# Kernel optimization log

Hardware: AMD Instinct MI355X
Metric: run time of the kernel (lower is better)

## Reference

```python
import jax, jax.numpy as jnp
import numpy as np

MAX_LEN, BATCH, EMB = 512, 32, 41
HID, UNITS = 800, 20
BOND_LENS = jnp.array([1.329, 1.459, 1.525], jnp.float32)
BOND_ANGLES = jnp.array([2.034, 2.119, 1.937], jnp.float32)
INIT_ABC = jnp.array([[0.0, 0.0, 1.0], [0.0, 1.0, 0.0], [1.0, 0.0, 0.0]], jnp.float32)


def _lstm_dir(x, w_ih, w_hh, b, reverse):
    # x: [T, B, in]; returns hidden states [T, B, H]
    T, B, _ = x.shape
    H = w_hh.shape[1]
    xs = jnp.flip(x, 0) if reverse else x
    xw = jnp.einsum('tbi,gi->tbg', xs, w_ih) + b  # precompute input projection

    def step(carry, xt):
        h, c = carry
        gates = xt + h @ w_hh.T
        i, f, g, o = jnp.split(gates, 4, axis=-1)
        c = jax.nn.sigmoid(f) * c + jax.nn.sigmoid(i) * jnp.tanh(g)
        h = jax.nn.sigmoid(o) * jnp.tanh(c)
        return (h, c), h

    init = (jnp.zeros((B, H), x.dtype), jnp.zeros((B, H), x.dtype))
    _, hs = jax.lax.scan(step, init, xw)
    return jnp.flip(hs, 0) if reverse else hs


def _bilstm_layer(x, w_ih, w_hh, b):
    # w_ih: [2, 4H, in]; w_hh: [2, 4H, H]; b: [2, 4H]
    fwd = _lstm_dir(x, w_ih[0], w_hh[0], b[0], False)
    bwd = _lstm_dir(x, w_ih[1], w_hh[1], b[1], True)
    return jnp.concatenate([fwd, bwd], axis=-1)


def _geometric_unit(coords3, triplet):
    # coords3: [3, B, 3] last three atoms; triplet: [B, 3] torsion angles
    A, Bc, C = coords3[0], coords3[1], coords3[2]
    new = []
    for i in range(3):
        Tang, R, P = BOND_ANGLES[i], BOND_LENS[i], triplet[:, i]
        D2 = jnp.stack([-R * jnp.cos(Tang) * jnp.ones_like(P),
                        R * jnp.cos(P) * jnp.sin(Tang),
                        R * jnp.sin(P) * jnp.sin(Tang)], axis=1)  # [B,3]
        BC = C - Bc
        bc = BC / jnp.linalg.norm(BC, axis=1, keepdims=True)
        AB = Bc - A
        N = jnp.cross(AB, bc)
        n = N / jnp.linalg.norm(N, axis=1, keepdims=True)
        M = jnp.stack([bc, jnp.cross(n, bc), n], axis=2)  # [B,3,3]
        D = jnp.einsum('bij,bj->bi', M, D2) + C
        A, Bc, C = Bc, C, D
        new.append(D)
    return jnp.stack([A, Bc, C]), jnp.stack(new)  # carry, [3,B,3]


def setup_inputs() -> dict:
    key = jax.random.key(0)
    ks = jax.random.split(key, 10)
    k = 1.0 / np.sqrt(HID)
    u = lambda kk, shp, lim: jax.random.uniform(kk, shp, jnp.float32, -lim, lim)
    in0, in1 = EMB + 1, 2 * HID
    return {
        'sequences': jax.random.normal(ks[0], (MAX_LEN, BATCH, EMB), jnp.float32),
        'lengths': jnp.full((BATCH,), MAX_LEN, jnp.int64 if jax.config.jax_enable_x64 else jnp.int32),
        'w_ih0': u(ks[1], (2, 4 * HID, in0), k),
        'w_hh0': u(ks[2], (2, 4 * HID, HID), k),
        'b0': u(ks[3], (2, 4 * HID), k),
        'w_ih1': u(ks[4], (2, 4 * HID, in1), k),
        'w_hh1': u(ks[5], (2, 4 * HID, HID), k),
        'b1': u(ks[6], (2, 4 * HID), k),
        'lin_w': u(ks[7], (UNITS, 2 * HID), 1.0 / np.sqrt(2 * HID)),
        'lin_b': u(ks[8], (UNITS,), 1.0 / np.sqrt(2 * HID)),
        'alphabet': jax.random.uniform(ks[9], (UNITS, 3), jnp.float32, -3.14, 3.14),
    }


def reference(sequences, lengths, w_ih0, w_hh0, b0, w_ih1, w_hh1, b1, lin_w, lin_b, alphabet):
    T, B, _ = sequences.shape
    abs_pos = jnp.broadcast_to(jnp.arange(T, dtype=sequences.dtype)[:, None, None], (T, B, 1))
    x = jnp.concatenate([sequences, abs_pos], axis=2)  # [T, B, EMB+1]
    # 2-layer bidirectional LSTM (all lengths == max_len -> packing is identity)
    h = _bilstm_layer(x, w_ih0, w_hh0, b0)
    h = _bilstm_layer(h, w_ih1, w_hh1, b1)  # [T, B, 2H]
    # linear -> softmax over alphabet, trig angle decode
    soft = jax.nn.softmax(h @ lin_w.T + lin_b, axis=2)  # [T, B, UNITS]
    sine = soft @ jnp.sin(alphabet)   # [T, B, 3]
    cosine = soft @ jnp.cos(alphabet)
    out = jnp.arctan2(sine, cosine)   # torsion angle triplets
    # sequential geometric coordinate recurrence over timesteps 1..T-1
    init = jnp.broadcast_to(INIT_ABC[:, None, :], (3, B, 3))
    _, new_coords = jax.lax.scan(_geometric_unit, init, out[1:])  # [T-1, 3, B, 3]
    pred_coords = jnp.concatenate([init, new_coords.reshape(-1, B, 3)], axis=0)
    return pred_coords  # [3 + 3*(T-1), B, 3]
```

## Files before the change

### kernel.cpp

```cpp
#include <hip/hip_runtime.h>
#include <math.h>

#define T_LEN 512
#define NB    32
#define EMB_  41
#define IN0_  42
#define HID_  800
#define G4_   3200
#define IN1_  1600
#define NU    20
#define NCH   100

typedef unsigned short u16;
typedef unsigned int   u32;
typedef unsigned long long u64;
typedef __attribute__((ext_vector_type(8))) short short8;
typedef __attribute__((ext_vector_type(4))) float f32x4;

__device__ __forceinline__ float bf2f(u16 v) {
    union { u32 u; float f; } c; c.u = ((u32)v) << 16; return c.f;
}
__device__ __forceinline__ u16 f2bf(float f) {
    union { float f; u32 u; } c; c.f = f;
    u32 r = (c.u + 0x7fffu + ((c.u >> 16) & 1u)) >> 16;
    return (u16)r;
}
__device__ __forceinline__ short cvt_hl(float v, int hl) {
    u16 hi = f2bf(v);
    return hl ? (short)f2bf(v - bf2f(hi)) : (short)hi;
}
__device__ __forceinline__ f32x4 mfma16(short8 a, short8 b, f32x4 c) {
    return __builtin_amdgcn_mfma_f32_16x16x32_bf16(a, b, c, 0, 0, 0);
}
__device__ __forceinline__ u64 aload(const u64* p) {
    return __hip_atomic_load(p, __ATOMIC_RELAXED, __HIP_MEMORY_SCOPE_AGENT);
}
__device__ __forceinline__ void astore(u64* p, u64 v) {
    __hip_atomic_store(p, v, __ATOMIC_RELAXED, __HIP_MEMORY_SCOPE_AGENT);
}
__device__ __forceinline__ int afload(const int* p) {
    return __hip_atomic_load(p, __ATOMIC_RELAXED, __HIP_MEMORY_SCOPE_AGENT);
}
__device__ __forceinline__ void afstore(int* p, int v) {
    __hip_atomic_store(p, v, __ATOMIC_RELAXED, __HIP_MEMORY_SCOPE_AGENT);
}

__global__ __launch_bounds__(256, 1)
void lstm0_persist(const float* __restrict__ seq, const float* __restrict__ wih0,
                   const float* __restrict__ whh0, const float* __restrict__ bias,
                   u16* __restrict__ h0f, u16* __restrict__ hB, int* __restrict__ flags)
{
    __shared__ __align__(16) float part[2048];
    __shared__ __align__(16) u16 stageB[25600];
    __shared__ __align__(16) float w0l[32*48];
    __shared__ __align__(16) float xsl[32*48];
    __shared__ u16 hpk[NB*8];
    const int tid = threadIdx.x;
    const int d = blockIdx.x / NCH, ch = blockIdx.x % NCH;
    const int w = tid >> 6, l = tid & 63;
    const int p = w & 1, hl = w >> 1;
    int* myflags = flags + d*NCH*16;

    short8 wreg[25];
    {
        const int m = l & 15, g = p*2 + (m>>3), j = ch*8 + (m&7);
        const float* base = whh0 + ((size_t)(d*G4_ + g*HID_ + j))*HID_ + (l>>4)*8;
#pragma unroll
        for (int kc = 0; kc < 25; ++kc) {
            float4 f0 = *(const float4*)(base + kc*32);
            float4 f1 = *(const float4*)(base + kc*32 + 4);
            short8 v;
            v[0]=cvt_hl(f0.x,hl); v[1]=cvt_hl(f0.y,hl); v[2]=cvt_hl(f0.z,hl); v[3]=cvt_hl(f0.w,hl);
            v[4]=cvt_hl(f1.x,hl); v[5]=cvt_hl(f1.y,hl); v[6]=cvt_hl(f1.z,hl); v[7]=cvt_hl(f1.w,hl);
            wreg[kc] = v;
        }
    }
    for (int idx = tid; idx < 32*EMB_; idx += 256) {
        int r = idx / EMB_, k = idx % EMB_;
        int ju_ = r >> 2, g = r & 3;
        w0l[r*48 + k] = wih0[((size_t)(d*G4_ + g*HID_ + ch*8 + ju_))*IN0_ + k];
    }
    const int ju = tid >> 5, b = tid & 31;
    const int j = ch*8 + ju;
    const int nt = b >> 4, n = b & 15;
    float biasr[4], wpos[4];
#pragma unroll
    for (int g = 0; g < 4; ++g) {
        biasr[g] = bias[d*G4_ + g*HID_ + j];
        wpos[g]  = wih0[((size_t)(d*G4_ + g*HID_ + j))*IN0_ + EMB_];
    }
    float creg = 0.f;
    __syncthreads();

    for (int s = 0; s < T_LEN; ++s) {
        const int t = d ? (T_LEN-1-s) : s;
        const u64* hq64 = (const u64*)(hB + (size_t)((s&1)*2 + d)*25600);
        u64*      hnq  = (u64*)(hB + (size_t)(((s&1)^1)*2 + d)*25600);

        if (s > 0 && tid < NCH)
            while (afload(myflags + tid*16) < s) __builtin_amdgcn_s_sleep(1);
        __syncthreads();

        {
            u64 tmp[25];
#pragma unroll
            for (int q = 0; q < 25; ++q) tmp[q] = aload(hq64 + tid + q*256);
#pragma unroll
            for (int q = 0; q < 25; ++q) ((u64*)stageB)[tid + q*256] = tmp[q];
        }
        for (int idx = tid; idx < 32*EMB_; idx += 256)
            xsl[(idx/EMB_)*48 + idx%EMB_] = seq[(size_t)t*(NB*EMB_) + idx];
        __syncthreads();

        f32x4 acc0 = {0.f,0.f,0.f,0.f}, acc1 = {0.f,0.f,0.f,0.f};
#pragma unroll 5
        for (int kc = 0; kc < 25; ++kc) {
            short8 b0 = *(const short8*)(stageB + kc*1024 + l*8);
            short8 b1 = *(const short8*)(stageB + kc*1024 + 512 + l*8);
            acc0 = mfma16(wreg[kc], b0, acc0);
            acc1 = mfma16(wreg[kc], b1, acc1);
        }
        {
            const int mrow = (l>>4)*4, nn = l & 15;
#pragma unroll
            for (int r = 0; r < 4; ++r) {
                part[(((p*2+hl)*2 + 0)*16 + mrow + r)*16 + nn] = acc0[r];
                part[(((p*2+hl)*2 + 1)*16 + mrow + r)*16 + nn] = acc1[r];
            }
        }
        __syncthreads();

        float dot0 = 0.f, dot1 = 0.f, dot2 = 0.f, dot3 = 0.f;
        {
            const float* wr = &w0l[ju*4*48];
            const float* xr = &xsl[b*48];
#pragma unroll
            for (int k4 = 0; k4 < 40; k4 += 4) {
                float4 xk = *(const float4*)(xr + k4);
                float4 w0 = *(const float4*)(wr + 0*48 + k4);
                float4 w1 = *(const float4*)(wr + 1*48 + k4);
                float4 w2 = *(const float4*)(wr + 2*48 + k4);
                float4 w3 = *(const float4*)(wr + 3*48 + k4);
                dot0 += w0.x*xk.x + w0.y*xk.y + w0.z*xk.z + w0.w*xk.w;
                dot1 += w1.x*xk.x + w1.y*xk.y + w1.z*xk.z + w1.w*xk.w;
                dot2 += w2.x*xk.x + w2.y*xk.y + w2.z*xk.z + w2.w*xk.w;
                dot3 += w3.x*xk.x + w3.y*xk.y + w3.z*xk.z + w3.w*xk.w;
            }
            float xk = xr[40];
            dot0 += wr[0*48+40]*xk; dot1 += wr[1*48+40]*xk;
            dot2 += wr[2*48+40]*xk; dot3 += wr[3*48+40]*xk;
        }
        float v[4] = {dot0, dot1, dot2, dot3};
#pragma unroll
        for (int g = 0; g < 4; ++g) {
            const int pp = g >> 1, m = (g & 1)*8 + ju;
            v[g] += part[(((pp*2+0)*2 + nt)*16 + m)*16 + n]
                  + part[(((pp*2+1)*2 + nt)*16 + m)*16 + n]
                  + biasr[g] + (float)t * wpos[g];
        }
        float ig = 1.f/(1.f + expf(-v[0]));
        float fg = 1.f/(1.f + expf(-v[1]));
        float gg = tanhf(v[2]);
        float og = 1.f/(1.f + expf(-v[3]));
        creg = fg * creg + ig * gg;
        hpk[b*8 + ju] = f2bf(og * tanhf(creg));
        __syncthreads();

        if (tid < 64) {
            const int bb = tid >> 1, half = tid & 1;
            const u16* hp = &hpk[bb*8 + half*4];
            u64 pk = (u64)hp[0] | ((u64)hp[1]<<16) | ((u64)hp[2]<<32) | ((u64)hp[3]<<48);
            const int ntb = bb >> 4, llb = ((ch&3)<<4) | (bb&15);
            astore(hnq + ((ch>>2)*2 + ntb)*128 + llb*2 + half, pk);
            u64* xq = (u64*)(h0f + (size_t)t*51200);
            xq[((d*25 + (ch>>2))*2 + ntb)*128 + llb*2 + half] = pk;
        }
        __syncthreads();
        if (tid == 0) afstore(myflags + ch*16, s+1);
    }
}

__global__ __launch_bounds__(256, 1)
void lstm1_persist(const float* __restrict__ wih1, const float* __restrict__ whh1,
                   const float* __restrict__ bias, const float* __restrict__ lin_w,
                   const u16* __restrict__ h0f, u16* __restrict__ hB,
                   int* __restrict__ flags, float* __restrict__ logits)
{
    __shared__ __align__(16) u16 wihL[2*50*512];
    __shared__ __align__(16) u16 stageB[25600];
    __shared__ float lwc[8*NU];
    __shared__ float hblk[8*NB];
    __shared__ u16 hpk[NB*8];
    float* part = (float*)stageB;
    const int tid = threadIdx.x;
    const int d = blockIdx.x / NCH, ch = blockIdx.x % NCH;
    const int w = tid >> 6, l = tid & 63;
    const int p = w & 1, hl = w >> 1;
    int* myflags = flags + d*NCH*16;

    short8 wreg[25];
    {
        const int m = l & 15, g = p*2 + (m>>3), j = ch*8 + (m&7);
        const float* base = whh1 + ((size_t)(d*G4_ + g*HID_ + j))*HID_ + (l>>4)*8;
#pragma unroll
        for (int kc = 0; kc < 25; ++kc) {
            float4 f0 = *(const float4*)(base + kc*32);
            float4 f1 = *(const float4*)(base + kc*32 + 4);
            short8 v;
            v[0]=cvt_hl(f0.x,hl); v[1]=cvt_hl(f0.y,hl); v[2]=cvt_hl(f0.z,hl); v[3]=cvt_hl(f0.w,hl);
            v[4]=cvt_hl(f1.x,hl); v[5]=cvt_hl(f1.y,hl); v[6]=cvt_hl(f1.z,hl); v[7]=cvt_hl(f1.w,hl);
            wreg[kc] = v;
        }
    }
    for (int o = tid; o < 6400; o += 256) {
        int pp = o / 3200, r = o % 3200, kc = r >> 6, ll = r & 63;
        int m = ll & 15, g = pp*2 + (m>>3), jj = ch*8 + (m&7);
        const float* base = wih1 + ((size_t)(d*G4_ + g*HID_ + jj))*IN1_ + kc*32 + (ll>>4)*8;
        float4 f0 = *(const float4*)base;
        float4 f1 = *(const float4*)(base + 4);
        short8 v;
        v[0]=(short)f2bf(f0.x); v[1]=(short)f2bf(f0.y); v[2]=(short)f2bf(f0.z); v[3]=(short)f2bf(f0.w);
        v[4]=(short)f2bf(f1.x); v[5]=(short)f2bf(f1.y); v[6]=(short)f2bf(f1.z); v[7]=(short)f2bf(f1.w);
        *(short8*)&wihL[o*8] = v;
    }
    if (tid < 8*NU) {
        int jju = tid / NU, u = tid % NU;
        lwc[tid] = lin_w[(size_t)u*IN1_ + d*HID_ + ch*8 + jju];
    }
    const int ju = tid >> 5, b = tid & 31;
    const int j = ch*8 + ju;
    const int nt = b >> 4, n = b & 15;
    float biasr[4];
#pragma unroll
    for (int g = 0; g < 4; ++g) biasr[g] = bias[d*G4_ + g*HID_ + j];
    float creg = 0.f;
    __syncthreads();

    for (int s = 0; s < T_LEN; ++s) {
        const int t = d ? (T_LEN-1-s) : s;
        const u64* hq64 = (const u64*)(hB + (size_t)((s&1)*2 + d)*25600);
        u64*      hnq  = (u64*)(hB + (size_t)(((s&1)^1)*2 + d)*25600);

        if (s > 0 && tid < NCH)
            while (afload(myflags + tid*16) < s) __builtin_amdgcn_s_sleep(1);
        __syncthreads();

        {
            u64 tmp[25];
#pragma unroll
            for (int q = 0; q < 25; ++q) tmp[q] = aload(hq64 + tid + q*256);
#pragma unroll
            for (int q = 0; q < 25; ++q) ((u64*)stageB)[tid + q*256] = tmp[q];
        }
        __syncthreads();

        f32x4 acc0 = {0.f,0.f,0.f,0.f}, acc1 = {0.f,0.f,0.f,0.f};
#pragma unroll 5
        for (int kc = 0; kc < 25; ++kc) {
            short8 b0 = *(const short8*)(stageB + kc*1024 + l*8);
            short8 b1 = *(const short8*)(stageB + kc*1024 + 512 + l*8);
            acc0 = mfma16(wreg[kc], b0, acc0);
            acc1 = mfma16(wreg[kc], b1, acc1);
        }
        const u16* xb = h0f + (size_t)t*51200;
#pragma unroll 5
        for (int kc = 0; kc < 25; ++kc) {
            const int idx = hl*25 + kc;
            short8 a  = *(const short8*)&wihL[(p*50 + idx)*512 + l*8];
            short8 b0 = *(const short8*)(xb + idx*1024 + l*8);
            short8 b1 = *(const short8*)(xb + idx*1024 + 512 + l*8);
            acc0 = mfma16(a, b0, acc0);
            acc1 = mfma16(a, b1, acc1);
        }
        __syncthreads();
        {
            const int mrow = (l>>4)*4, nn = l & 15;
#pragma unroll
            for (int r = 0; r < 4; ++r) {
                part[(((p*2+hl)*2 + 0)*16 + mrow + r)*16 + nn] = acc0[r];
                part[(((p*2+hl)*2 + 1)*16 + mrow + r)*16 + nn] = acc1[r];
            }
        }
        __syncthreads();

        float v[4];
#pragma unroll
        for (int g = 0; g < 4; ++g) {
            const int pp = g >> 1, m = (g & 1)*8 + ju;
            v[g] = part[(((pp*2+0)*2 + nt)*16 + m)*16 + n]
                 + part[(((pp*2+1)*2 + nt)*16 + m)*16 + n] + biasr[g];
        }
        float ig = 1.f/(1.f + expf(-v[0]));
        float fg = 1.f/(1.f + expf(-v[1]));
        float gg = tanhf(v[2]);
        float og = 1.f/(1.f + expf(-v[3]));
        creg = fg * creg + ig * gg;
        float hn = og * tanhf(creg);
        hblk[ju*NB + b] = hn;
        hpk[b*8 + ju] = f2bf(hn);
        __syncthreads();

        if (tid < 64) {
            const int bb = tid >> 1, half = tid & 1;
            const u16* hp = &hpk[bb*8 + half*4];
            u64 pk = (u64)hp[0] | ((u64)hp[1]<<16) | ((u64)hp[2]<<32) | ((u64)hp[3]<<48);
            const int ntb = bb >> 4, llb = ((ch&3)<<4) | (bb&15);
            astore(hnq + ((ch>>2)*2 + ntb)*128 + llb*2 + half, pk);
        }
        __syncthreads();
        if (tid == 0) afstore(myflags + ch*16, s+1);

        {
            float* lg = logits + (size_t)t*(NB*NU);
            for (int q = tid; q < NB*NU; q += 256) {
                int kk = q + (ch & 31)*NU;
                if (kk >= NB*NU) kk -= NB*NU;
                const int bb = kk / NU, uu = kk % NU;
                float sum = 0.f;
#pragma unroll
                for (int qq = 0; qq < 8; ++qq) sum += lwc[qq*NU + uu] * hblk[qq*NB + bb];
                atomicAdd(lg + kk, sum);
            }
        }
    }
}

__global__ __launch_bounds__(256) void logits_init(const float* __restrict__ lb, float* __restrict__ logits)
{
    int idx = blockIdx.x * 256 + threadIdx.x;
    if (idx < T_LEN*NB*NU) logits[idx] = lb[idx % NU];
}

__global__ __launch_bounds__(256)
void epilogue(const float* __restrict__ logits, const float* __restrict__ alphabet,
              float* __restrict__ cs)
{
    __shared__ float sa[NU*3], ca[NU*3];
    const int tid = threadIdx.x;
    if (tid < NU*3) { float al = alphabet[tid]; sa[tid] = sinf(al); ca[tid] = cosf(al); }
    __syncthreads();
    const int row = blockIdx.x*256 + tid;
    if (row >= T_LEN*NB) return;
    float lg[NU];
    float m = -1e30f;
#pragma unroll 4
    for (int u = 0; u < NU; ++u) { lg[u] = logits[(size_t)row*NU + u]; m = fmaxf(m, lg[u]); }
    float ssum = 0.f;
#pragma unroll 4
    for (int u = 0; u < NU; ++u) { lg[u] = expf(lg[u] - m); ssum += lg[u]; }
    float inv = 1.f / ssum;
#pragma unroll
    for (int i = 0; i < 3; ++i) {
        float sv = 0.f, cv = 0.f;
#pragma unroll 4
        for (int u = 0; u < NU; ++u) {
            float sw = lg[u] * inv;
            sv += sw * sa[u*3 + i];
            cv += sw * ca[u*3 + i];
        }
        float rinv = rsqrtf(fmaxf(sv*sv + cv*cv, 1e-30f));
        *(float2*)(cs + ((size_t)row*3 + i)*2) = make_float2(cv*rinv, sv*rinv);
    }
}

__global__ __launch_bounds__(64)
void geometry(const float* __restrict__ cs, float* __restrict__ out)
{
    const int b = threadIdx.x;
    if (b >= NB) return;
    const float blen[3] = {1.329f, 1.459f, 1.525f};
    const float bang[3] = {2.034f, 2.119f, 1.937f};
    float sT[3], cT[3];
#pragma unroll
    for (int i = 0; i < 3; ++i) { sT[i] = sinf(bang[i]); cT[i] = cosf(bang[i]); }

    float Ax=0.f,Ay=0.f,Az=1.f, Bx=0.f,By=1.f,Bz=0.f, Cx=1.f,Cy=0.f,Cz=0.f;
    out[(0*NB + b)*3 + 0] = 0.f; out[(0*NB + b)*3 + 1] = 0.f; out[(0*NB + b)*3 + 2] = 1.f;
    out[(1*NB + b)*3 + 0] = 0.f; out[(1*NB + b)*3 + 1] = 1.f; out[(1*NB + b)*3 + 2] = 0.f;
    out[(2*NB + b)*3 + 0] = 1.f; out[(2*NB + b)*3 + 1] = 0.f; out[(2*NB + b)*3 + 2] = 0.f;

    for (int t = 1; t < T_LEN; ++t) {
        float2 pc[3];
#pragma unroll
        for (int i = 0; i < 3; ++i)
            pc[i] = *(const float2*)(cs + (((size_t)t*NB + b)*3 + i)*2);
#pragma unroll
        for (int i = 0; i < 3; ++i) {
            float R = blen[i];
            float d2x = -R*cT[i], d2y = R*pc[i].x*sT[i], d2z = R*pc[i].y*sT[i];
            float bcx = Cx-Bx, bcy = Cy-By, bcz = Cz-Bz;
            float inv = rsqrtf(bcx*bcx + bcy*bcy + bcz*bcz);
            bcx *= inv; bcy *= inv; bcz *= inv;
            float abx = Bx-Ax, aby = By-Ay, abz = Bz-Az;
            float nx = aby*bcz - abz*bcy;
            float ny = abz*bcx - abx*bcz;
            float nz = abx*bcy - aby*bcx;
            inv = rsqrtf(fmaxf(nx*nx + ny*ny + nz*nz, 1e-30f));
            nx *= inv; ny *= inv; nz *= inv;
            float mx = ny*bcz - nz*bcy;
            float my = nz*bcx - nx*bcz;
            float mz = nx*bcy - ny*bcx;
            float Dx = bcx*d2x + mx*d2y + nx*d2z + Cx;
            float Dy = bcy*d2x + my*d2y + ny*d2z + Cy;
            float Dz = bcz*d2x + mz*d2y + nz*d2z + Cz;
            Ax=Bx; Ay=By; Az=Bz; Bx=Cx; By=Cy; Bz=Cz; Cx=Dx; Cy=Dy; Cz=Dz;
            const int r = 3 + (t-1)*3 + i;
            out[((size_t)r*NB + b)*3 + 0] = Dx;
            out[((size_t)r*NB + b)*3 + 1] = Dy;
            out[((size_t)r*NB + b)*3 + 2] = Dz;
        }
    }
}

extern "C" void kernel_launch(void* const* d_in, const int* in_sizes, int n_in,
                              void* d_out, int out_size, void* d_ws, size_t ws_size,
                              hipStream_t stream)
{
    (void)in_sizes; (void)n_in; (void)out_size; (void)ws_size;
    const float* seq   = (const float*)d_in[0];
    const float* w_ih0 = (const float*)d_in[2];
    const float* w_hh0 = (const float*)d_in[3];
    const float* b0    = (const float*)d_in[4];
    const float* w_ih1 = (const float*)d_in[5];
    const float* w_hh1 = (const float*)d_in[6];
    const float* b1    = (const float*)d_in[7];
    const float* lin_w = (const float*)d_in[8];
    const float* lin_b = (const float*)d_in[9];
    const float* alpha = (const float*)d_in[10];

    char* ws = (char*)d_ws;
    size_t off = 0;
    u16* h0f   = (u16*)(ws + off); off += 52428800ull;
    u16* hB    = (u16*)(ws + off); off += 204800ull;
    int* flagsL0 = (int*)(ws + off); off += 12800ull;
    int* flagsL1 = (int*)(ws + off); off += 12800ull;
    float* logits = (float*)(ws + off); off += 1310720ull;
    float* cs = (float*)(ws + off); off += 393216ull;

    hipMemsetAsync(hB, 0, 204800 + 12800 + 12800, stream);
    logits_init<<<dim3(1280), dim3(256), 0, stream>>>(lin_b, logits);

    lstm0_persist<<<dim3(2*NCH), dim3(256), 0, stream>>>(seq, w_ih0, w_hh0, b0, h0f, hB, flagsL0);

    hipMemsetAsync(hB, 0, 204800, stream);
    lstm1_persist<<<dim3(2*NCH), dim3(256), 0, stream>>>(w_ih1, w_hh1, b1, lin_w, h0f, hB,
                                                         flagsL1, logits);

    epilogue<<<dim3(64), dim3(256), 0, stream>>>(logits, alpha, cs);
    geometry<<<dim3(1), dim3(64), 0, stream>>>(cs, (float*)d_out);
}
```

Baseline: 10.86 ms.

## Hoist recurrence-independent work off the LSTM critical path and replicate logits accumulators

In layer 0, the input-slice load now happens before the spin-wait, and the h0f global store moves after the flag release. In layer 1, the input-projection MFMA loop (which does not depend on the previous hidden state) now runs before waiting on the other blocks' flags, so it overlaps the inter-block synchronisation. Logits atomics are spread over 8 replicated buffers to cut atomic contention, and the epilogue sums them and adds the bias. This costs a larger memset and extra epilogue reads.

```diff
diff --git a/kernel.cpp b/kernel.cpp
--- a/kernel.cpp
+++ b/kernel.cpp
@@ -10,6 +10,7 @@
 #define IN1_  1600
 #define NU    20
 #define NCH   100
+#define NREP  8
 
 typedef unsigned short u16;
 typedef unsigned int   u32;
@@ -97,6 +98,9 @@
         const u64* hq64 = (const u64*)(hB + (size_t)((s&1)*2 + d)*25600);
         u64*      hnq  = (u64*)(hB + (size_t)(((s&1)^1)*2 + d)*25600);
 
+        for (int idx = tid; idx < 32*EMB_; idx += 256)
+            xsl[(idx/EMB_)*48 + idx%EMB_] = seq[(size_t)t*(NB*EMB_) + idx];
+
         if (s > 0 && tid < NCH)
             while (afload(myflags + tid*16) < s) __builtin_amdgcn_s_sleep(1);
         __syncthreads();
@@ -108,8 +112,6 @@
 #pragma unroll
             for (int q = 0; q < 25; ++q) ((u64*)stageB)[tid + q*256] = tmp[q];
         }
-        for (int idx = tid; idx < 32*EMB_; idx += 256)
-            xsl[(idx/EMB_)*48 + idx%EMB_] = seq[(size_t)t*(NB*EMB_) + idx];
         __syncthreads();
 
         f32x4 acc0 = {0.f,0.f,0.f,0.f}, acc1 = {0.f,0.f,0.f,0.f};
@@ -166,17 +168,19 @@
         hpk[b*8 + ju] = f2bf(og * tanhf(creg));
         __syncthreads();
 
+        u64 pk = 0; int xoff = 0;
         if (tid < 64) {
             const int bb = tid >> 1, half = tid & 1;
             const u16* hp = &hpk[bb*8 + half*4];
-            u64 pk = (u64)hp[0] | ((u64)hp[1]<<16) | ((u64)hp[2]<<32) | ((u64)hp[3]<<48);
+            pk = (u64)hp[0] | ((u64)hp[1]<<16) | ((u64)hp[2]<<32) | ((u64)hp[3]<<48);
             const int ntb = bb >> 4, llb = ((ch&3)<<4) | (bb&15);
             astore(hnq + ((ch>>2)*2 + ntb)*128 + llb*2 + half, pk);
-            u64* xq = (u64*)(h0f + (size_t)t*51200);
-            xq[((d*25 + (ch>>2))*2 + ntb)*128 + llb*2 + half] = pk;
+            xoff = ((d*25 + (ch>>2))*2 + ntb)*128 + llb*2 + half;
         }
         __syncthreads();
         if (tid == 0) afstore(myflags + ch*16, s+1);
+        if (tid < 64)
+            ((u64*)(h0f + (size_t)t*51200))[xoff] = pk;
     }
 }
 
@@ -234,6 +238,7 @@
 #pragma unroll
     for (int g = 0; g < 4; ++g) biasr[g] = bias[d*G4_ + g*HID_ + j];
     float creg = 0.f;
+    float* lrep = logits + (size_t)(ch & (NREP-1)) * (T_LEN*NB*NU);
     __syncthreads();
 
     for (int s = 0; s < T_LEN; ++s) {
@@ -241,6 +246,20 @@
         const u64* hq64 = (const u64*)(hB + (size_t)((s&1)*2 + d)*25600);
         u64*      hnq  = (u64*)(hB + (size_t)(((s&1)^1)*2 + d)*25600);
 
+        f32x4 acc0 = {0.f,0.f,0.f,0.f}, acc1 = {0.f,0.f,0.f,0.f};
+        {
+            const u16* xb = h0f + (size_t)t*51200;
+#pragma unroll 5
+            for (int kc = 0; kc < 25; ++kc) {
+                const int idx = hl*25 + kc;
+                short8 a  = *(const short8*)&wihL[(p*50 + idx)*512 + l*8];
+                short8 b0 = *(const short8*)(xb + idx*1024 + l*8);
+                short8 b1 = *(const short8*)(xb + idx*1024 + 512 + l*8);
+                acc0 = mfma16(a, b0, acc0);
+                acc1 = mfma16(a, b1, acc1);
+            }
+        }
+
         if (s > 0 && tid < NCH)
             while (afload(myflags + tid*16) < s) __builtin_amdgcn_s_sleep(1);
         __syncthreads();
@@ -254,23 +273,12 @@
         }
         __syncthreads();
 
-        f32x4 acc0 = {0.f,0.f,0.f,0.f}, acc1 = {0.f,0.f,0.f,0.f};
 #pragma unroll 5
         for (int kc = 0; kc < 25; ++kc) {
             short8 b0 = *(const short8*)(stageB + kc*1024 + l*8);
             short8 b1 = *(const short8*)(stageB + kc*1024 + 512 + l*8);
             acc0 = mfma16(wreg[kc], b0, acc0);
             acc1 = mfma16(wreg[kc], b1, acc1);
-        }
-        const u16* xb = h0f + (size_t)t*51200;
-#pragma unroll 5
-        for (int kc = 0; kc < 25; ++kc) {
-            const int idx = hl*25 + kc;
-            short8 a  = *(const short8*)&wihL[(p*50 + idx)*512 + l*8];
-            short8 b0 = *(const short8*)(xb + idx*1024 + l*8);
-            short8 b1 = *(const short8*)(xb + idx*1024 + 512 + l*8);
-            acc0 = mfma16(a, b0, acc0);
-            acc1 = mfma16(a, b1, acc1);
         }
         __syncthreads();
         {
@@ -311,7 +319,7 @@
         if (tid == 0) afstore(myflags + ch*16, s+1);
 
         {
-            float* lg = logits + (size_t)t*(NB*NU);
+            float* lg = lrep + (size_t)t*(NB*NU);
             for (int q = tid; q < NB*NU; q += 256) {
                 int kk = q + (ch & 31)*NU;
                 if (kk >= NB*NU) kk -= NB*NU;
@@ -325,26 +333,28 @@
     }
 }
 
-__global__ __launch_bounds__(256) void logits_init(const float* __restrict__ lb, float* __restrict__ logits)
+__global__ __launch_bounds__(256)
+void epilogue(const float* __restrict__ logits, const float* __restrict__ lin_b,
+              const float* __restrict__ alphabet, float* __restrict__ cs)
 {
-    int idx = blockIdx.x * 256 + threadIdx.x;
-    if (idx < T_LEN*NB*NU) logits[idx] = lb[idx % NU];
-}
-
-__global__ __launch_bounds__(256)
-void epilogue(const float* __restrict__ logits, const float* __restrict__ alphabet,
-              float* __restrict__ cs)
-{
-    __shared__ float sa[NU*3], ca[NU*3];
+    __shared__ float sa[NU*3], ca[NU*3], lb[NU];
     const int tid = threadIdx.x;
     if (tid < NU*3) { float al = alphabet[tid]; sa[tid] = sinf(al); ca[tid] = cosf(al); }
+    if (tid < NU) lb[tid] = lin_b[tid];
     __syncthreads();
     const int row = blockIdx.x*256 + tid;
     if (row >= T_LEN*NB) return;
     float lg[NU];
+#pragma unroll 4
+    for (int u = 0; u < NU; ++u) lg[u] = lb[u];
+    for (int r = 0; r < NREP; ++r) {
+        const float* lp = logits + (size_t)r*(T_LEN*NB*NU) + (size_t)row*NU;
+#pragma unroll 4
+        for (int u = 0; u < NU; ++u) lg[u] += lp[u];
+    }
     float m = -1e30f;
 #pragma unroll 4
-    for (int u = 0; u < NU; ++u) { lg[u] = logits[(size_t)row*NU + u]; m = fmaxf(m, lg[u]); }
+    for (int u = 0; u < NU; ++u) m = fmaxf(m, lg[u]);
     float ssum = 0.f;
 #pragma unroll 4
     for (int u = 0; u < NU; ++u) { lg[u] = expf(lg[u] - m); ssum += lg[u]; }
@@ -434,11 +444,11 @@
     u16* hB    = (u16*)(ws + off); off += 204800ull;
     int* flagsL0 = (int*)(ws + off); off += 12800ull;
     int* flagsL1 = (int*)(ws + off); off += 12800ull;
-    float* logits = (float*)(ws + off); off += 1310720ull;
+    float* logits = (float*)(ws + off); off += (size_t)NREP*1310720ull;
     float* cs = (float*)(ws + off); off += 393216ull;
 
     hipMemsetAsync(hB, 0, 204800 + 12800 + 12800, stream);
-    logits_init<<<dim3(1280), dim3(256), 0, stream>>>(lin_b, logits);
+    hipMemsetAsync(logits, 0, (size_t)NREP*1310720ull, stream);
 
     lstm0_persist<<<dim3(2*NCH), dim3(256), 0, stream>>>(seq, w_ih0, w_hh0, b0, h0f, hB, flagsL0);
 
@@ -446,6 +456,6 @@
     lstm1_persist<<<dim3(2*NCH), dim3(256), 0, stream>>>(w_ih1, w_hh1, b1, lin_w, h0f, hB,
                                                          flagsL1, logits);
 
-    epilogue<<<dim3(64), dim3(256), 0, stream>>>(logits, alpha, cs);
+    epilogue<<<dim3(64), dim3(256), 0, stream>>>(logits, lin_b, alpha, cs);
     geometry<<<dim3(1), dim3(64), 0, stream>>>(cs, (float*)d_out);
 }
```

Measured after the change: 9.664 ms. 1.12x faster.
